# Kernel optimization log

Hardware: AMD Instinct MI355X
Metric: run time of the kernel (lower is better)

Reference implementation:

```python
import jax, jax.numpy as jnp
import numpy as np

K_VALS = 3
N_FEATURES = 128


def setup_inputs() -> dict:
    key = jax.random.key(0)
    x = jax.random.normal(key, (8, 256, 256, 256), dtype=jnp.float32)  # [B, C, H, W]
    return {"x": x}


def reference(x):
    B, C, H, W = x.shape
    # channel-last, topk over channels: [B,H,W,k]
    xl = jnp.transpose(x, (0, 2, 3, 1))
    topk_v, topk_i = jax.lax.top_k(xl, K_VALS)
    # back to [B, k, H, W]
    topk_v = jnp.transpose(topk_v, (0, 3, 1, 2))
    topk_i = jnp.transpose(topk_i, (0, 3, 1, 2))
    # MaxPool3d(kernel=(3,1,1), stride=1, ceil_mode=True) on [B,k=3,H,W]
    # collapses the k dim to 1 (single window covering all 3 values).
    max_vals = jnp.max(topk_v, axis=1).reshape(B, H * W)  # [B, H*W]
    _, idxn = jax.lax.top_k(max_vals, N_FEATURES)  # [B, n_features]
    flat_topk = topk_v.reshape(B, K_VALS, H * W)
    flat_idxk = topk_i.reshape(B, K_VALS, H * W)
    gather_idx = idxn[:, None, :]  # [B,1,nf] broadcast over k
    reduced_topk = jnp.take_along_axis(flat_topk, gather_idx, axis=2)  # [B,k,nf]
    reduced_idxk = jnp.take_along_axis(flat_idxk, gather_idx, axis=2).astype(jnp.float32)
    idxn_out = idxn[:, None, :]  # matches torch [B,1,nf]
    return (reduced_idxk, reduced_topk, idxn_out)
```

## Files before the change

### kernel.cpp

```cpp
#include <hip/hip_runtime.h>
#include <hip/hip_bf16.h>
#include <float.h>

#define NB 8
#define NC 256
#define HW 65536
#define KV 3
#define NF 128

__device__ __forceinline__ unsigned mono(float f) {
    unsigned u = __float_as_uint(f);
    return (u & 0x80000000u) ? ~u : (u | 0x80000000u);
}

__global__ __launch_bounds__(256) void chan_max_kernel(
    const float* __restrict__ x, unsigned* __restrict__ keys) {
    size_t t = (size_t)blockIdx.x * 256 + threadIdx.x;
    int b = (int)(t >> 14);
    int g = (int)(t & 16383);
    const float4* px = (const float4*)(x + (size_t)b * NC * HW) + g;
    float m0 = -FLT_MAX, m1 = -FLT_MAX, m2 = -FLT_MAX, m3 = -FLT_MAX;
#pragma unroll 8
    for (int c = 0; c < NC; ++c) {
        float4 v = px[(size_t)c * (HW / 4)];
        m0 = fmaxf(m0, v.x);
        m1 = fmaxf(m1, v.y);
        m2 = fmaxf(m2, v.z);
        m3 = fmaxf(m3, v.w);
    }
    uint4 kk;
    kk.x = mono(m0); kk.y = mono(m1); kk.z = mono(m2); kk.w = mono(m3);
    ((uint4*)keys)[t] = kk;
}

__global__ __launch_bounds__(1024) void topk_select_kernel(
    const unsigned* __restrict__ keys, int* __restrict__ sel,
    float* __restrict__ out_idxn) {
    int b = blockIdx.x;
    const unsigned* kb = keys + (size_t)b * HW;
    int tid = threadIdx.x;

    __shared__ unsigned hist[256];
    __shared__ unsigned sh_thresh, sh_krem;
    __shared__ unsigned cand_key[256];
    __shared__ int cand_idx[256];
    __shared__ int eq_idx[512];
    __shared__ int n_gt, n_eq;

    if (tid == 0) { sh_thresh = 0u; sh_krem = NF; }

    for (int shift = 24; shift >= 0; shift -= 8) {
        if (tid < 256) hist[tid] = 0u;
        __syncthreads();
        unsigned thresh = sh_thresh;
        unsigned mask = (shift == 24) ? 0u : (0xFFFFFFFFu << (shift + 8));
        for (int i = tid; i < HW; i += 1024) {
            unsigned k = kb[i];
            if ((k & mask) == thresh)
                atomicAdd(&hist[(k >> shift) & 255], 1u);
        }
        __syncthreads();
        if (tid == 0) {
            unsigned krem = sh_krem;
            unsigned cum = 0;
            int bsel = 0;
            for (int bin = 255; bin >= 0; --bin) {
                if (cum + hist[bin] >= krem) { bsel = bin; break; }
                cum += hist[bin];
            }
            sh_thresh = thresh | ((unsigned)bsel << shift);
            sh_krem = krem - cum;
        }
        __syncthreads();
    }

    unsigned T = sh_thresh;
    int krem = (int)sh_krem;
    if (tid == 0) { n_gt = 0; n_eq = 0; }
    __syncthreads();

    for (int i = tid; i < HW; i += 1024) {
        unsigned k = kb[i];
        if (k > T) {
            int pos = atomicAdd(&n_gt, 1);
            if (pos < 256) { cand_key[pos] = k; cand_idx[pos] = i; }
        } else if (k == T) {
            int pos = atomicAdd(&n_eq, 1);
            if (pos < 512) eq_idx[pos] = i;
        }
    }
    __syncthreads();

    int ngt = n_gt;
    int neq = min(n_eq, 512);
    if (tid < neq) {
        int my = eq_idx[tid];
        int r = 0;
        for (int j = 0; j < neq; ++j)
            if (eq_idx[j] < my) r++;
        if (r < krem) { cand_key[ngt + r] = T; cand_idx[ngt + r] = my; }
    }
    __syncthreads();

    if (tid < NF) {
        unsigned mk = cand_key[tid];
        int mi = cand_idx[tid];
        int r = 0;
        for (int j = 0; j < NF; ++j) {
            unsigned k2 = cand_key[j];
            int i2 = cand_idx[j];
            if (k2 > mk || (k2 == mk && i2 < mi)) r++;
        }
        sel[b * NF + r] = mi;
        out_idxn[b * NF + r] = (float)mi;
    }
}

__device__ __forceinline__ void ins3(float v, int c,
                                     float& v0, int& c0,
                                     float& v1, int& c1,
                                     float& v2, int& c2) {
    bool b0 = (v > v0) || (v == v0 && c < c0);
    bool b1 = (v > v1) || (v == v1 && c < c1);
    bool b2 = (v > v2) || (v == v2 && c < c2);
    if (b0) { v2 = v1; c2 = c1; v1 = v0; c1 = c0; v0 = v; c0 = c; }
    else if (b1) { v2 = v1; c2 = c1; v1 = v; c1 = c; }
    else if (b2) { v2 = v; c2 = c; }
}

__global__ __launch_bounds__(256) void gather_top3_kernel(
    const float* __restrict__ x, const int* __restrict__ sel,
    float* __restrict__ out_idxk, float* __restrict__ out_topk) {
    int gtid = blockIdx.x * 256 + threadIdx.x;
    int wid = gtid >> 6;
    int lane = threadIdx.x & 63;
    int b = wid >> 7;
    int n = wid & 127;
    int p = sel[b * NF + n];

    const float* xb = x + (size_t)b * NC * HW + p;
    float v0 = -FLT_MAX, v1 = -FLT_MAX, v2 = -FLT_MAX;
    int c0 = 0x7FFFFFFF, c1 = 0x7FFFFFFF, c2 = 0x7FFFFFFF;
#pragma unroll
    for (int j = 0; j < 4; ++j) {
        int c = lane + j * 64;
        float v = xb[(size_t)c * HW];
        ins3(v, c, v0, c0, v1, c1, v2, c2);
    }
#pragma unroll
    for (int off = 1; off < 64; off <<= 1) {
        float w0 = __shfl_xor(v0, off);
        float w1 = __shfl_xor(v1, off);
        float w2 = __shfl_xor(v2, off);
        int d0 = __shfl_xor(c0, off);
        int d1 = __shfl_xor(c1, off);
        int d2 = __shfl_xor(c2, off);
        ins3(w0, d0, v0, c0, v1, c1, v2, c2);
        ins3(w1, d1, v0, c0, v1, c1, v2, c2);
        ins3(w2, d2, v0, c0, v1, c1, v2, c2);
    }
    if (lane == 0) {
        size_t base = (size_t)b * (KV * NF) + n;
        out_topk[base]            = v0;
        out_topk[base + NF]       = v1;
        out_topk[base + 2 * NF]   = v2;
        out_idxk[base]            = (float)c0;
        out_idxk[base + NF]       = (float)c1;
        out_idxk[base + 2 * NF]   = (float)c2;
    }
}

extern "C" void kernel_launch(void* const* d_in, const int* in_sizes, int n_in,
                              void* d_out, int out_size, void* d_ws, size_t ws_size,
                              hipStream_t stream) {
    const float* x = (const float*)d_in[0];
    float* out = (float*)d_out;
    float* out_idxk = out;
    float* out_topk = out + NB * KV * NF;
    float* out_idxn = out + 2 * NB * KV * NF;

    unsigned* keys = (unsigned*)d_ws;
    int* sel = (int*)((char*)d_ws + (size_t)NB * HW * 4);

    chan_max_kernel<<<dim3(NB * HW / 4 / 256), dim3(256), 0, stream>>>(x, keys);
    topk_select_kernel<<<dim3(NB), dim3(1024), 0, stream>>>(keys, sel, out_idxn);
    gather_top3_kernel<<<dim3(NB * NF / 4), dim3(256), 0, stream>>>(x, sel, out_idxk, out_topk);
}
```

Before: 828.3 us.

## Compute per-pixel top-3 in the channel scan and drop the gather kernel

The channel-reduction kernel now keeps a full top-3 (values and channel indices) per pixel instead of just the max, and writes them to workspace. The selection kernel then reads these for the 128 chosen pixels, so the separate strided gather kernel goes away. The radix-select histogram gains a wave-uniform atomic fast path and a parallel suffix scan in place of the serial thread-0 bin search. The price is more compare/select ALU work per element and four times the workspace writes in the bandwidth-bound first pass.

```diff
diff --git a/kernel.cpp b/kernel.cpp
--- a/kernel.cpp
+++ b/kernel.cpp
@@ -12,39 +12,77 @@
     unsigned u = __float_as_uint(f);
     return (u & 0x80000000u) ? ~u : (u | 0x80000000u);
 }
-
-__global__ __launch_bounds__(256) void chan_max_kernel(
-    const float* __restrict__ x, unsigned* __restrict__ keys) {
-    size_t t = (size_t)blockIdx.x * 256 + threadIdx.x;
-    int b = (int)(t >> 14);
-    int g = (int)(t & 16383);
-    const float4* px = (const float4*)(x + (size_t)b * NC * HW) + g;
-    float m0 = -FLT_MAX, m1 = -FLT_MAX, m2 = -FLT_MAX, m3 = -FLT_MAX;
-#pragma unroll 8
-    for (int c = 0; c < NC; ++c) {
-        float4 v = px[(size_t)c * (HW / 4)];
-        m0 = fmaxf(m0, v.x);
-        m1 = fmaxf(m1, v.y);
-        m2 = fmaxf(m2, v.z);
-        m3 = fmaxf(m3, v.w);
-    }
-    uint4 kk;
-    kk.x = mono(m0); kk.y = mono(m1); kk.z = mono(m2); kk.w = mono(m3);
-    ((uint4*)keys)[t] = kk;
+__device__ __forceinline__ float demono(unsigned k) {
+    unsigned u = (k & 0x80000000u) ? (k ^ 0x80000000u) : ~k;
+    return __uint_as_float(u);
 }
 
-__global__ __launch_bounds__(1024) void topk_select_kernel(
-    const unsigned* __restrict__ keys, int* __restrict__ sel,
-    float* __restrict__ out_idxn) {
+__global__ __launch_bounds__(256) void top3_kernel(
+    const float* __restrict__ x,
+    uint4* __restrict__ k0p, uint4* __restrict__ k1p,
+    uint4* __restrict__ k2p, uint4* __restrict__ chp)
+{
+    unsigned t = blockIdx.x * 256 + threadIdx.x;
+    int b = t >> 14;
+    int g = t & 16383;
+    const float4* px = (const float4*)(x + (size_t)b * NC * HW) + g;
+
+    float v0[4], v1[4], v2[4];
+    int c0[4], c1[4], c2[4];
+#pragma unroll
+    for (int j = 0; j < 4; ++j) {
+        v0[j] = v1[j] = v2[j] = -FLT_MAX;
+        c0[j] = c1[j] = c2[j] = 0;
+    }
+
+#pragma unroll 4
+    for (int c = 0; c < NC; ++c) {
+        float4 val = px[(size_t)c * (HW / 4)];
+        float vv[4] = {val.x, val.y, val.z, val.w};
+#pragma unroll
+        for (int j = 0; j < 4; ++j) {
+            float v = vv[j];
+            bool b0 = v > v0[j], b1 = v > v1[j], b2 = v > v2[j];
+            float nv2 = b1 ? v1[j] : (b2 ? v : v2[j]);
+            int   nc2 = b1 ? c1[j] : (b2 ? c : c2[j]);
+            float nv1 = b0 ? v0[j] : (b1 ? v : v1[j]);
+            int   nc1 = b0 ? c0[j] : (b1 ? c : c1[j]);
+            float nv0 = b0 ? v : v0[j];
+            int   nc0 = b0 ? c : c0[j];
+            v2[j] = nv2; c2[j] = nc2;
+            v1[j] = nv1; c1[j] = nc1;
+            v0[j] = nv0; c0[j] = nc0;
+        }
+    }
+
+    uint4 o0, o1, o2, oc;
+    o0.x = mono(v0[0]); o0.y = mono(v0[1]); o0.z = mono(v0[2]); o0.w = mono(v0[3]);
+    o1.x = mono(v1[0]); o1.y = mono(v1[1]); o1.z = mono(v1[2]); o1.w = mono(v1[3]);
+    o2.x = mono(v2[0]); o2.y = mono(v2[1]); o2.z = mono(v2[2]); o2.w = mono(v2[3]);
+    oc.x = (unsigned)c0[0] | ((unsigned)c1[0] << 8) | ((unsigned)c2[0] << 16);
+    oc.y = (unsigned)c0[1] | ((unsigned)c1[1] << 8) | ((unsigned)c2[1] << 16);
+    oc.z = (unsigned)c0[2] | ((unsigned)c1[2] << 8) | ((unsigned)c2[2] << 16);
+    oc.w = (unsigned)c0[3] | ((unsigned)c1[3] << 8) | ((unsigned)c2[3] << 16);
+    k0p[t] = o0; k1p[t] = o1; k2p[t] = o2; chp[t] = oc;
+}
+
+__global__ __launch_bounds__(1024) void select_kernel(
+    const unsigned* __restrict__ k0p, const unsigned* __restrict__ k1p,
+    const unsigned* __restrict__ k2p, const unsigned* __restrict__ chp,
+    float* __restrict__ out_idxk, float* __restrict__ out_topk,
+    float* __restrict__ out_idxn)
+{
     int b = blockIdx.x;
-    const unsigned* kb = keys + (size_t)b * HW;
+    const unsigned* kb = k0p + (size_t)b * HW;
     int tid = threadIdx.x;
+    int lane = tid & 63;
 
     __shared__ unsigned hist[256];
+    __shared__ unsigned suf[256];
     __shared__ unsigned sh_thresh, sh_krem;
     __shared__ unsigned cand_key[256];
     __shared__ int cand_idx[256];
-    __shared__ int eq_idx[512];
+    __shared__ int eq_idx[1024];
     __shared__ int n_gt, n_eq;
 
     if (tid == 0) { sh_thresh = 0u; sh_krem = NF; }
@@ -53,23 +91,37 @@
         if (tid < 256) hist[tid] = 0u;
         __syncthreads();
         unsigned thresh = sh_thresh;
+        unsigned krem = sh_krem;
         unsigned mask = (shift == 24) ? 0u : (0xFFFFFFFFu << (shift + 8));
         for (int i = tid; i < HW; i += 1024) {
             unsigned k = kb[i];
-            if ((k & mask) == thresh)
-                atomicAdd(&hist[(k >> shift) & 255], 1u);
+            bool ok = ((k & mask) == thresh);
+            unsigned bin = (k >> shift) & 255u;
+            unsigned long long ball = __ballot(ok);
+            unsigned fb = __shfl(bin, 0);
+            bool uni = (ball == ~0ULL) && __all(bin == fb);
+            if (uni) {
+                if (lane == 0) atomicAdd(&hist[fb], 64u);
+            } else if (ok) {
+                atomicAdd(&hist[bin], 1u);
+            }
         }
         __syncthreads();
-        if (tid == 0) {
-            unsigned krem = sh_krem;
-            unsigned cum = 0;
-            int bsel = 0;
-            for (int bin = 255; bin >= 0; --bin) {
-                if (cum + hist[bin] >= krem) { bsel = bin; break; }
-                cum += hist[bin];
+        if (tid < 256) suf[tid] = hist[tid];
+        __syncthreads();
+        for (int off = 1; off < 256; off <<= 1) {
+            unsigned add = 0;
+            if (tid < 256 && tid + off < 256) add = suf[tid + off];
+            __syncthreads();
+            if (tid < 256) suf[tid] += add;
+            __syncthreads();
+        }
+        if (tid < 256) {
+            unsigned cum = (tid == 255) ? 0u : suf[tid + 1];
+            if (cum < krem && suf[tid] >= krem) {
+                sh_thresh = thresh | ((unsigned)tid << shift);
+                sh_krem = krem - cum;
             }
-            sh_thresh = thresh | ((unsigned)bsel << shift);
-            sh_krem = krem - cum;
         }
         __syncthreads();
     }
@@ -86,13 +138,13 @@
             if (pos < 256) { cand_key[pos] = k; cand_idx[pos] = i; }
         } else if (k == T) {
             int pos = atomicAdd(&n_eq, 1);
-            if (pos < 512) eq_idx[pos] = i;
+            if (pos < 1024) eq_idx[pos] = i;
         }
     }
     __syncthreads();
 
     int ngt = n_gt;
-    int neq = min(n_eq, 512);
+    int neq = min(n_eq, 1024);
     if (tid < neq) {
         int my = eq_idx[tid];
         int r = 0;
@@ -111,62 +163,18 @@
             int i2 = cand_idx[j];
             if (k2 > mk || (k2 == mk && i2 < mi)) r++;
         }
-        sel[b * NF + r] = mi;
+        size_t pix = (size_t)b * HW + mi;
+        unsigned kk1 = k1p[pix];
+        unsigned kk2 = k2p[pix];
+        unsigned ch = chp[pix];
         out_idxn[b * NF + r] = (float)mi;
-    }
-}
-
-__device__ __forceinline__ void ins3(float v, int c,
-                                     float& v0, int& c0,
-                                     float& v1, int& c1,
-                                     float& v2, int& c2) {
-    bool b0 = (v > v0) || (v == v0 && c < c0);
-    bool b1 = (v > v1) || (v == v1 && c < c1);
-    bool b2 = (v > v2) || (v == v2 && c < c2);
-    if (b0) { v2 = v1; c2 = c1; v1 = v0; c1 = c0; v0 = v; c0 = c; }
-    else if (b1) { v2 = v1; c2 = c1; v1 = v; c1 = c; }
-    else if (b2) { v2 = v; c2 = c; }
-}
-
-__global__ __launch_bounds__(256) void gather_top3_kernel(
-    const float* __restrict__ x, const int* __restrict__ sel,
-    float* __restrict__ out_idxk, float* __restrict__ out_topk) {
-    int gtid = blockIdx.x * 256 + threadIdx.x;
-    int wid = gtid >> 6;
-    int lane = threadIdx.x & 63;
-    int b = wid >> 7;
-    int n = wid & 127;
-    int p = sel[b * NF + n];
-
-    const float* xb = x + (size_t)b * NC * HW + p;
-    float v0 = -FLT_MAX, v1 = -FLT_MAX, v2 = -FLT_MAX;
-    int c0 = 0x7FFFFFFF, c1 = 0x7FFFFFFF, c2 = 0x7FFFFFFF;
-#pragma unroll
-    for (int j = 0; j < 4; ++j) {
-        int c = lane + j * 64;
-        float v = xb[(size_t)c * HW];
-        ins3(v, c, v0, c0, v1, c1, v2, c2);
-    }
-#pragma unroll
-    for (int off = 1; off < 64; off <<= 1) {
-        float w0 = __shfl_xor(v0, off);
-        float w1 = __shfl_xor(v1, off);
-        float w2 = __shfl_xor(v2, off);
-        int d0 = __shfl_xor(c0, off);
-        int d1 = __shfl_xor(c1, off);
-        int d2 = __shfl_xor(c2, off);
-        ins3(w0, d0, v0, c0, v1, c1, v2, c2);
-        ins3(w1, d1, v0, c0, v1, c1, v2, c2);
-        ins3(w2, d2, v0, c0, v1, c1, v2, c2);
-    }
-    if (lane == 0) {
-        size_t base = (size_t)b * (KV * NF) + n;
-        out_topk[base]            = v0;
-        out_topk[base + NF]       = v1;
-        out_topk[base + 2 * NF]   = v2;
-        out_idxk[base]            = (float)c0;
-        out_idxk[base + NF]       = (float)c1;
-        out_idxk[base + 2 * NF]   = (float)c2;
+        size_t ob = (size_t)b * KV * NF + r;
+        out_topk[ob]          = demono(mk);
+        out_topk[ob + NF]     = demono(kk1);
+        out_topk[ob + 2 * NF] = demono(kk2);
+        out_idxk[ob]          = (float)(ch & 255u);
+        out_idxk[ob + NF]     = (float)((ch >> 8) & 255u);
+        out_idxk[ob + 2 * NF] = (float)((ch >> 16) & 255u);
     }
 }
 
@@ -179,10 +187,13 @@
     float* out_topk = out + NB * KV * NF;
     float* out_idxn = out + 2 * NB * KV * NF;
 
-    unsigned* keys = (unsigned*)d_ws;
-    int* sel = (int*)((char*)d_ws + (size_t)NB * HW * 4);
+    unsigned* k0p = (unsigned*)d_ws;
+    unsigned* k1p = k0p + (size_t)NB * HW;
+    unsigned* k2p = k1p + (size_t)NB * HW;
+    unsigned* chp = k2p + (size_t)NB * HW;
 
-    chan_max_kernel<<<dim3(NB * HW / 4 / 256), dim3(256), 0, stream>>>(x, keys);
-    topk_select_kernel<<<dim3(NB), dim3(1024), 0, stream>>>(keys, sel, out_idxn);
-    gather_top3_kernel<<<dim3(NB * NF / 4), dim3(256), 0, stream>>>(x, sel, out_idxk, out_topk);
+    top3_kernel<<<dim3(NB * HW / 4 / 256), dim3(256), 0, stream>>>(
+        x, (uint4*)k0p, (uint4*)k1p, (uint4*)k2p, (uint4*)chp);
+    select_kernel<<<dim3(NB), dim3(1024), 0, stream>>>(
+        k0p, k1p, k2p, chp, out_idxk, out_topk, out_idxn);
 }
```

Result: faster. 786.8 us (-5.0%).
